# Kernel tuning notes

Measured on AMD Instinct MI355X. Metric: run time of the kernel, lower is better.

## Reference

```python
import jax, jax.numpy as jnp
import numpy as np

BN_EPS = 1e-5
LEAKY_SLOPE = 0.01

N_TOTAL, FEAT_DIM = 100000, 128
N_BATCH, K = 50000, 16
EMBED_DIM = 128


def setup_inputs() -> dict:
    key = jax.random.key(0)
    k1, k2, k3 = jax.random.split(key, 3)
    raw_features = jax.random.normal(k1, (N_TOTAL, FEAT_DIM), dtype=jnp.float32)
    weight = jax.random.normal(k2, (FEAT_DIM, EMBED_DIM), dtype=jnp.float32) * (1.0 / np.sqrt(FEAT_DIM))
    gamma = jnp.ones((EMBED_DIM,), dtype=jnp.float32)
    beta = jnp.zeros((EMBED_DIM,), dtype=jnp.float32)
    neigh_idx = jax.random.randint(k3, (N_BATCH, K), 0, N_TOTAL, dtype=jnp.int64)
    return {"raw_features": raw_features, "weight": weight, "gamma": gamma,
            "beta": beta, "neigh_idx": neigh_idx}


def reference(raw_features, weight, gamma, beta, neigh_idx):
    # Mean aggregation over sampled neighbors: [N_BATCH, K, F] -> [N_BATCH, F]
    neigh_feats = jnp.mean(raw_features[neigh_idx], axis=1)
    # Dense transform: [N_BATCH, EMBED_DIM]
    x = neigh_feats @ weight
    # BatchNorm1d (training mode: batch statistics, biased variance)
    mean = jnp.mean(x, axis=0)
    var = jnp.var(x, axis=0)
    x = (x - mean) * jax.lax.rsqrt(var + BN_EPS) * gamma + beta
    # LeakyReLU (default negative_slope=0.01)
    return jnp.where(x >= 0, x, LEAKY_SLOPE * x)
```

## Files before the change

kernel.cpp:

```cpp
#include <hip/hip_runtime.h>
#include <hip/hip_bf16.h>


#define NTOTAL 100000
#define FEAT   128
#define NB     50000
#define KNEI   16
#define NTILES (NB / 16)

typedef float f32x4 __attribute__((ext_vector_type(4)));
typedef short bf16x8 __attribute__((ext_vector_type(8)));

__device__ __forceinline__ unsigned short f2bf(float f) {
    union { float f; unsigned u; } v; v.f = f;
    unsigned r = v.u + 0x7FFF + ((v.u >> 16) & 1);
    return (unsigned short)(r >> 16);
}

#define WT_LD 136
#define A_LD  136

__global__ __launch_bounds__(256, 4) void enc_gemm(
    const float* __restrict__ raw, const float* __restrict__ W,
    const int* __restrict__ idx, float* __restrict__ out,
    float* __restrict__ gstats)
{
    __shared__ unsigned short sWt[128 * WT_LD];
    __shared__ unsigned short sA[16 * A_LD];
    __shared__ int sidx[256];

    const int t = threadIdx.x;

    #pragma unroll 4
    for (int i = 0; i < 64; ++i) {
        int e = t + i * 256;
        int f = e >> 7, n = e & 127;
        sWt[n * WT_LD + f] = f2bf(W[e]);
    }

    const int lane = t & 63;
    const int wv = t >> 6;
    const int ln = lane & 15;
    const int qd = lane >> 4;
    const int c = t & 31;
    const int g = t >> 5;

    float s1a = 0.f, s2a = 0.f, s1b = 0.f, s2b = 0.f;
    const float4* raw4 = (const float4*)raw;

    for (int tile = blockIdx.x; tile < NTILES; tile += gridDim.x) {
        const int i0 = tile * 16;
        __syncthreads();
        sidx[t] = idx[i0 * KNEI + t];
        __syncthreads();

        #pragma unroll
        for (int rr = 0; rr < 2; ++rr) {
            const int r = g * 2 + rr;
            const int* ip = &sidx[r * KNEI];
            float4 acc = {0.f, 0.f, 0.f, 0.f};
            #pragma unroll
            for (int k = 0; k < KNEI; ++k) {
                float4 v = raw4[(size_t)ip[k] * 32 + c];
                acc.x += v.x; acc.y += v.y; acc.z += v.z; acc.w += v.w;
            }
            ushort4 b;
            b.x = f2bf(acc.x * 0.0625f); b.y = f2bf(acc.y * 0.0625f);
            b.z = f2bf(acc.z * 0.0625f); b.w = f2bf(acc.w * 0.0625f);
            *(ushort4*)&sA[r * A_LD + c * 4] = b;
        }
        __syncthreads();

        f32x4 acc0 = {0.f, 0.f, 0.f, 0.f}, acc1 = {0.f, 0.f, 0.f, 0.f};
        const int n0 = wv * 32 + ln, n1 = n0 + 16;
        #pragma unroll
        for (int kt = 0; kt < 4; ++kt) {
            const int k0 = kt * 32 + qd * 8;
            bf16x8 a  = *(const bf16x8*)&sA[ln * A_LD + k0];
            bf16x8 b0 = *(const bf16x8*)&sWt[n0 * WT_LD + k0];
            bf16x8 b1 = *(const bf16x8*)&sWt[n1 * WT_LD + k0];
            acc0 = __builtin_amdgcn_mfma_f32_16x16x32_bf16(a, b0, acc0, 0, 0, 0);
            acc1 = __builtin_amdgcn_mfma_f32_16x16x32_bf16(a, b1, acc1, 0, 0, 0);
        }

        #pragma unroll
        for (int ri = 0; ri < 4; ++ri) {
            const int row = i0 + qd * 4 + ri;
            float v0 = acc0[ri], v1 = acc1[ri];
            out[row * FEAT + n0] = v0;
            out[row * FEAT + n1] = v1;
            s1a += v0; s2a += v0 * v0;
            s1b += v1; s2b += v1 * v1;
        }
    }

    s1a += __shfl_down(s1a, 32); s1a += __shfl_down(s1a, 16);
    s2a += __shfl_down(s2a, 32); s2a += __shfl_down(s2a, 16);
    s1b += __shfl_down(s1b, 32); s1b += __shfl_down(s1b, 16);
    s2b += __shfl_down(s2b, 32); s2b += __shfl_down(s2b, 16);
    if ((lane >> 4) == 0) {
        const int n0 = wv * 32 + ln, n1 = n0 + 16;
        atomicAdd(&gstats[n0], s1a);
        atomicAdd(&gstats[FEAT + n0], s2a);
        atomicAdd(&gstats[n1], s1b);
        atomicAdd(&gstats[FEAT + n1], s2b);
    }
}

__global__ __launch_bounds__(256) void enc_bn(
    float* __restrict__ out, const float* __restrict__ gstats,
    const float* __restrict__ gamma, const float* __restrict__ beta)
{
    __shared__ float sScale[FEAT], sShift[FEAT];
    const int t = threadIdx.x;
    if (t < FEAT) {
        float s1 = gstats[t], s2 = gstats[FEAT + t];
        float mean = s1 * (1.0f / NB);
        float var = s2 * (1.0f / NB) - mean * mean;
        float sc = gamma[t] * rsqrtf(var + 1e-5f);
        sScale[t] = sc;
        sShift[t] = beta[t] - mean * sc;
    }
    __syncthreads();

    const int total4 = NB * FEAT / 4;
    float4* o4 = (float4*)out;
    for (int e = blockIdx.x * blockDim.x + t; e < total4; e += gridDim.x * blockDim.x) {
        const int f4 = (e & 31) * 4;
        float4 v = o4[e];
        float4 r;
        float y;
        y = v.x * sScale[f4 + 0] + sShift[f4 + 0]; r.x = (y >= 0.f) ? y : 0.01f * y;
        y = v.y * sScale[f4 + 1] + sShift[f4 + 1]; r.y = (y >= 0.f) ? y : 0.01f * y;
        y = v.z * sScale[f4 + 2] + sShift[f4 + 2]; r.z = (y >= 0.f) ? y : 0.01f * y;
        y = v.w * sScale[f4 + 3] + sShift[f4 + 3]; r.w = (y >= 0.f) ? y : 0.01f * y;
        o4[e] = r;
    }
}

extern "C" void kernel_launch(void* const* d_in, const int* in_sizes, int n_in,
                              void* d_out, int out_size, void* d_ws, size_t ws_size,
                              hipStream_t stream) {
    const float* raw   = (const float*)d_in[0];
    const float* W     = (const float*)d_in[1];
    const float* gamma = (const float*)d_in[2];
    const float* beta  = (const float*)d_in[3];
    const int*   idx   = (const int*)d_in[4];
    float* out = (float*)d_out;
    float* gstats = (float*)d_ws;

    hipMemsetAsync(gstats, 0, 2 * FEAT * sizeof(float), stream);
    enc_gemm<<<1024, 256, 0, stream>>>(raw, W, idx, out, gstats);
    enc_bn<<<1024, 256, 0, stream>>>(out, gstats, gamma, beta);
}
```

Baseline: 162.5 us.

## Keep weight fragments in registers, batch gather loads, hoist BN scale

The bf16 weight tile moves out of a 34 KB shared-memory buffer into per-thread register fragments loaded straight from global memory. This cuts LDS use and should allow more resident blocks per CU. The neighbor gather now issues 8 loads at once into two accumulators to expose memory-level parallelism, and the grid grows to 1563 blocks so each block handles about two tiles. The BN kernel hoists per-thread scale and shift into registers, since each thread's feature column stays fixed across its grid-stride loop. In exchange, the per-thread weight loads are strided and uncoalesced and are repeated by every block, and register pressure rises.

Result: slower. 177.5 us (+9.2%).

```diff
diff --git a/kernel.cpp b/kernel.cpp
--- a/kernel.cpp
+++ b/kernel.cpp
@@ -7,6 +7,7 @@
 #define NB     50000
 #define KNEI   16
 #define NTILES (NB / 16)
+#define GRID_A 1563
 
 typedef float f32x4 __attribute__((ext_vector_type(4)));
 typedef short bf16x8 __attribute__((ext_vector_type(8)));
@@ -17,7 +18,6 @@
     return (unsigned short)(r >> 16);
 }
 
-#define WT_LD 136
 #define A_LD  136
 
 __global__ __launch_bounds__(256, 4) void enc_gemm(
@@ -25,25 +25,28 @@
     const int* __restrict__ idx, float* __restrict__ out,
     float* __restrict__ gstats)
 {
-    __shared__ unsigned short sWt[128 * WT_LD];
     __shared__ unsigned short sA[16 * A_LD];
     __shared__ int sidx[256];
 
     const int t = threadIdx.x;
-
-    #pragma unroll 4
-    for (int i = 0; i < 64; ++i) {
-        int e = t + i * 256;
-        int f = e >> 7, n = e & 127;
-        sWt[n * WT_LD + f] = f2bf(W[e]);
-    }
-
     const int lane = t & 63;
     const int wv = t >> 6;
     const int ln = lane & 15;
     const int qd = lane >> 4;
     const int c = t & 31;
     const int g = t >> 5;
+
+    const int n0 = wv * 32 + ln, n1 = n0 + 16;
+    bf16x8 bf0[4], bf1[4];
+    #pragma unroll
+    for (int kt = 0; kt < 4; ++kt) {
+        const int k0 = kt * 32 + qd * 8;
+        #pragma unroll
+        for (int j = 0; j < 8; ++j) {
+            bf0[kt][j] = (short)f2bf(W[(k0 + j) * FEAT + n0]);
+            bf1[kt][j] = (short)f2bf(W[(k0 + j) * FEAT + n1]);
+        }
+    }
 
     float s1a = 0.f, s2a = 0.f, s1b = 0.f, s2b = 0.f;
     const float4* raw4 = (const float4*)raw;
@@ -58,29 +61,37 @@
         for (int rr = 0; rr < 2; ++rr) {
             const int r = g * 2 + rr;
             const int* ip = &sidx[r * KNEI];
-            float4 acc = {0.f, 0.f, 0.f, 0.f};
+            float4 v[8];
+            float ax = 0.f, ay = 0.f, az = 0.f, aw = 0.f;
+            float bx = 0.f, by = 0.f, bz = 0.f, bw = 0.f;
             #pragma unroll
-            for (int k = 0; k < KNEI; ++k) {
-                float4 v = raw4[(size_t)ip[k] * 32 + c];
-                acc.x += v.x; acc.y += v.y; acc.z += v.z; acc.w += v.w;
+            for (int k = 0; k < 8; ++k) v[k] = raw4[(size_t)ip[k] * 32 + c];
+            #pragma unroll
+            for (int k = 0; k < 8; k += 2) {
+                ax += v[k].x;   ay += v[k].y;   az += v[k].z;   aw += v[k].w;
+                bx += v[k+1].x; by += v[k+1].y; bz += v[k+1].z; bw += v[k+1].w;
+            }
+            #pragma unroll
+            for (int k = 0; k < 8; ++k) v[k] = raw4[(size_t)ip[k + 8] * 32 + c];
+            #pragma unroll
+            for (int k = 0; k < 8; k += 2) {
+                ax += v[k].x;   ay += v[k].y;   az += v[k].z;   aw += v[k].w;
+                bx += v[k+1].x; by += v[k+1].y; bz += v[k+1].z; bw += v[k+1].w;
             }
             ushort4 b;
-            b.x = f2bf(acc.x * 0.0625f); b.y = f2bf(acc.y * 0.0625f);
-            b.z = f2bf(acc.z * 0.0625f); b.w = f2bf(acc.w * 0.0625f);
+            b.x = f2bf((ax + bx) * 0.0625f); b.y = f2bf((ay + by) * 0.0625f);
+            b.z = f2bf((az + bz) * 0.0625f); b.w = f2bf((aw + bw) * 0.0625f);
             *(ushort4*)&sA[r * A_LD + c * 4] = b;
         }
         __syncthreads();
 
         f32x4 acc0 = {0.f, 0.f, 0.f, 0.f}, acc1 = {0.f, 0.f, 0.f, 0.f};
-        const int n0 = wv * 32 + ln, n1 = n0 + 16;
         #pragma unroll
         for (int kt = 0; kt < 4; ++kt) {
             const int k0 = kt * 32 + qd * 8;
-            bf16x8 a  = *(const bf16x8*)&sA[ln * A_LD + k0];
-            bf16x8 b0 = *(const bf16x8*)&sWt[n0 * WT_LD + k0];
-            bf16x8 b1 = *(const bf16x8*)&sWt[n1 * WT_LD + k0];
-            acc0 = __builtin_amdgcn_mfma_f32_16x16x32_bf16(a, b0, acc0, 0, 0, 0);
-            acc1 = __builtin_amdgcn_mfma_f32_16x16x32_bf16(a, b1, acc1, 0, 0, 0);
+            bf16x8 a = *(const bf16x8*)&sA[ln * A_LD + k0];
+            acc0 = __builtin_amdgcn_mfma_f32_16x16x32_bf16(a, bf0[kt], acc0, 0, 0, 0);
+            acc1 = __builtin_amdgcn_mfma_f32_16x16x32_bf16(a, bf1[kt], acc1, 0, 0, 0);
         }
 
         #pragma unroll
@@ -98,8 +109,7 @@
     s2a += __shfl_down(s2a, 32); s2a += __shfl_down(s2a, 16);
     s1b += __shfl_down(s1b, 32); s1b += __shfl_down(s1b, 16);
     s2b += __shfl_down(s2b, 32); s2b += __shfl_down(s2b, 16);
-    if ((lane >> 4) == 0) {
-        const int n0 = wv * 32 + ln, n1 = n0 + 16;
+    if (qd == 0) {
         atomicAdd(&gstats[n0], s1a);
         atomicAdd(&gstats[FEAT + n0], s2a);
         atomicAdd(&gstats[n1], s1b);
@@ -123,17 +133,20 @@
     }
     __syncthreads();
 
+    const int f4 = (t & 31) * 4;
+    const float4 sc = *(const float4*)&sScale[f4];
+    const float4 sh = *(const float4*)&sShift[f4];
+
     const int total4 = NB * FEAT / 4;
     float4* o4 = (float4*)out;
     for (int e = blockIdx.x * blockDim.x + t; e < total4; e += gridDim.x * blockDim.x) {
-        const int f4 = (e & 31) * 4;
         float4 v = o4[e];
         float4 r;
         float y;
-        y = v.x * sScale[f4 + 0] + sShift[f4 + 0]; r.x = (y >= 0.f) ? y : 0.01f * y;
-        y = v.y * sScale[f4 + 1] + sShift[f4 + 1]; r.y = (y >= 0.f) ? y : 0.01f * y;
-        y = v.z * sScale[f4 + 2] + sShift[f4 + 2]; r.z = (y >= 0.f) ? y : 0.01f * y;
-        y = v.w * sScale[f4 + 3] + sShift[f4 + 3]; r.w = (y >= 0.f) ? y : 0.01f * y;
+        y = v.x * sc.x + sh.x; r.x = (y >= 0.f) ? y : 0.01f * y;
+        y = v.y * sc.y + sh.y; r.y = (y >= 0.f) ? y : 0.01f * y;
+        y = v.z * sc.z + sh.z; r.z = (y >= 0.f) ? y : 0.01f * y;
+        y = v.w * sc.w + sh.w; r.w = (y >= 0.f) ? y : 0.01f * y;
         o4[e] = r;
     }
 }
@@ -150,6 +163,6 @@
     float* gstats = (float*)d_ws;
 
     hipMemsetAsync(gstats, 0, 2 * FEAT * sizeof(float), stream);
-    enc_gemm<<<1024, 256, 0, stream>>>(raw, W, idx, out, gstats);
+    enc_gemm<<<GRID_A, 256, 0, stream>>>(raw, W, idx, out, gstats);
     enc_bn<<<1024, 256, 0, stream>>>(out, gstats, gamma, beta);
 }
```

## Pre-convert features to bf16 and store intermediate GEMM output as bf16

Applied to the files above, without the earlier changes.

Adds a conversion kernel that casts the full raw feature table and the weight to bf16 in workspace, so the neighbor gather reads half the bytes per row. The GEMM writes its pre-BN output as bf16 to workspace, and the BN kernel reads it back and writes fp32, halving the intermediate round trip. The memset is folded into the conversion kernel. The cost is an extra full pass over the 51 MB feature table, a dependence on workspace size with a fallback path, and extra rounding from summing bf16 inputs.

After: 151.9 us. -6.5%, faster.

```diff
diff --git a/kernel.cpp b/kernel.cpp
--- a/kernel.cpp
+++ b/kernel.cpp
@@ -8,6 +8,12 @@
 #define KNEI   16
 #define NTILES (NB / 16)
 
+#define OFF_STATS 0
+#define OFF_WT    1024
+#define OFF_RAWB  33792
+#define OFF_XB    (33792 + 25600000)
+#define WS_NEEDED (OFF_XB + 12800000)
+
 typedef float f32x4 __attribute__((ext_vector_type(4)));
 typedef short bf16x8 __attribute__((ext_vector_type(8)));
 
@@ -20,7 +26,165 @@
 #define WT_LD 136
 #define A_LD  136
 
-__global__ __launch_bounds__(256, 4) void enc_gemm(
+__global__ __launch_bounds__(256) void enc_conv(
+    const float* __restrict__ raw, const float* __restrict__ W,
+    unsigned short* __restrict__ rawb, unsigned short* __restrict__ Wt,
+    float* __restrict__ gstats)
+{
+    const int t = threadIdx.x;
+    if (blockIdx.x < 64) {
+        int e = blockIdx.x * 256 + t;
+        int n = e >> 7, k = e & 127;
+        Wt[e] = f2bf(W[k * FEAT + n]);
+    }
+    if (blockIdx.x == 64 && t < 2 * FEAT) gstats[t] = 0.f;
+
+    const float4* raw4 = (const float4*)raw;
+    ushort4* rb4 = (ushort4*)rawb;
+    const int NQ = NTOTAL * FEAT / 4;
+    for (int e = blockIdx.x * 256 + t; e < NQ; e += gridDim.x * 256) {
+        float4 v = raw4[e];
+        ushort4 b;
+        b.x = f2bf(v.x); b.y = f2bf(v.y); b.z = f2bf(v.z); b.w = f2bf(v.w);
+        rb4[e] = b;
+    }
+}
+
+__global__ __launch_bounds__(256, 4) void enc_gemm_b(
+    const unsigned short* __restrict__ rawb, const unsigned short* __restrict__ Wt,
+    const int* __restrict__ idx, unsigned short* __restrict__ xb,
+    float* __restrict__ gstats)
+{
+    __shared__ unsigned short sWt[128 * WT_LD];
+    __shared__ unsigned short sA[16 * A_LD];
+    __shared__ int sidx[256];
+
+    const int t = threadIdx.x;
+
+    #pragma unroll
+    for (int i = 0; i < 8; ++i) {
+        int e = t + i * 256;
+        int n = e >> 4, c = e & 15;
+        *(uint4*)&sWt[n * WT_LD + c * 8] = *(const uint4*)&Wt[n * 128 + c * 8];
+    }
+
+    const int lane = t & 63;
+    const int wv = t >> 6;
+    const int ln = lane & 15;
+    const int qd = lane >> 4;
+    const int c2 = t & 15;
+    const int g  = t >> 4;
+    const int n0 = wv * 32 + ln, n1 = n0 + 16;
+
+    float s1a = 0.f, s2a = 0.f, s1b = 0.f, s2b = 0.f;
+
+    for (int tile = blockIdx.x; tile < NTILES; tile += gridDim.x) {
+        const int i0 = tile * 16;
+        __syncthreads();
+        sidx[t] = idx[i0 * KNEI + t];
+        __syncthreads();
+
+        {
+            const int* ip = &sidx[g * KNEI];
+            uint4 v[16];
+            #pragma unroll
+            for (int k = 0; k < KNEI; ++k)
+                v[k] = *(const uint4*)&rawb[(size_t)ip[k] * FEAT + c2 * 8];
+            float a0=0.f,a1=0.f,a2=0.f,a3=0.f,a4=0.f,a5=0.f,a6=0.f,a7=0.f;
+            #pragma unroll
+            for (int k = 0; k < KNEI; ++k) {
+                a0 += __uint_as_float(v[k].x << 16);
+                a1 += __uint_as_float(v[k].x & 0xFFFF0000u);
+                a2 += __uint_as_float(v[k].y << 16);
+                a3 += __uint_as_float(v[k].y & 0xFFFF0000u);
+                a4 += __uint_as_float(v[k].z << 16);
+                a5 += __uint_as_float(v[k].z & 0xFFFF0000u);
+                a6 += __uint_as_float(v[k].w << 16);
+                a7 += __uint_as_float(v[k].w & 0xFFFF0000u);
+            }
+            uint4 b;
+            b.x = (unsigned)f2bf(a0 * 0.0625f) | ((unsigned)f2bf(a1 * 0.0625f) << 16);
+            b.y = (unsigned)f2bf(a2 * 0.0625f) | ((unsigned)f2bf(a3 * 0.0625f) << 16);
+            b.z = (unsigned)f2bf(a4 * 0.0625f) | ((unsigned)f2bf(a5 * 0.0625f) << 16);
+            b.w = (unsigned)f2bf(a6 * 0.0625f) | ((unsigned)f2bf(a7 * 0.0625f) << 16);
+            *(uint4*)&sA[g * A_LD + c2 * 8] = b;
+        }
+        __syncthreads();
+
+        f32x4 acc0 = {0.f, 0.f, 0.f, 0.f}, acc1 = {0.f, 0.f, 0.f, 0.f};
+        #pragma unroll
+        for (int kt = 0; kt < 4; ++kt) {
+            const int k0 = kt * 32 + qd * 8;
+            bf16x8 a  = *(const bf16x8*)&sA[ln * A_LD + k0];
+            bf16x8 b0 = *(const bf16x8*)&sWt[n0 * WT_LD + k0];
+            bf16x8 b1 = *(const bf16x8*)&sWt[n1 * WT_LD + k0];
+            acc0 = __builtin_amdgcn_mfma_f32_16x16x32_bf16(a, b0, acc0, 0, 0, 0);
+            acc1 = __builtin_amdgcn_mfma_f32_16x16x32_bf16(a, b1, acc1, 0, 0, 0);
+        }
+
+        #pragma unroll
+        for (int ri = 0; ri < 4; ++ri) {
+            const int row = i0 + qd * 4 + ri;
+            float v0 = acc0[ri], v1 = acc1[ri];
+            xb[row * FEAT + n0] = f2bf(v0);
+            xb[row * FEAT + n1] = f2bf(v1);
+            s1a += v0; s2a += v0 * v0;
+            s1b += v1; s2b += v1 * v1;
+        }
+    }
+
+    s1a += __shfl_down(s1a, 32); s1a += __shfl_down(s1a, 16);
+    s2a += __shfl_down(s2a, 32); s2a += __shfl_down(s2a, 16);
+    s1b += __shfl_down(s1b, 32); s1b += __shfl_down(s1b, 16);
+    s2b += __shfl_down(s2b, 32); s2b += __shfl_down(s2b, 16);
+    if (qd == 0) {
+        atomicAdd(&gstats[n0], s1a);
+        atomicAdd(&gstats[FEAT + n0], s2a);
+        atomicAdd(&gstats[n1], s1b);
+        atomicAdd(&gstats[FEAT + n1], s2b);
+    }
+}
+
+__global__ __launch_bounds__(256) void enc_bn_b(
+    const unsigned short* __restrict__ xb, float* __restrict__ out,
+    const float* __restrict__ gstats,
+    const float* __restrict__ gamma, const float* __restrict__ beta)
+{
+    __shared__ float sScale[FEAT], sShift[FEAT];
+    const int t = threadIdx.x;
+    if (t < FEAT) {
+        float s1 = gstats[t], s2 = gstats[FEAT + t];
+        float mean = s1 * (1.0f / NB);
+        float var = s2 * (1.0f / NB) - mean * mean;
+        float sc = gamma[t] * rsqrtf(var + 1e-5f);
+        sScale[t] = sc;
+        sShift[t] = beta[t] - mean * sc;
+    }
+    __syncthreads();
+
+    const int f8 = (t & 15) * 8;
+    const float4 sc0 = *(const float4*)&sScale[f8], sc1 = *(const float4*)&sScale[f8 + 4];
+    const float4 sh0 = *(const float4*)&sShift[f8], sh1 = *(const float4*)&sShift[f8 + 4];
+
+    const uint4* x4 = (const uint4*)xb;
+    float4* o4 = (float4*)out;
+    const int total8 = NB * FEAT / 8;
+    for (int e = blockIdx.x * 256 + t; e < total8; e += gridDim.x * 256) {
+        uint4 v = x4[e];
+        float4 r0, r1; float y;
+        y = __uint_as_float(v.x << 16)        * sc0.x + sh0.x; r0.x = (y >= 0.f) ? y : 0.01f * y;
+        y = __uint_as_float(v.x & 0xFFFF0000u)* sc0.y + sh0.y; r0.y = (y >= 0.f) ? y : 0.01f * y;
+        y = __uint_as_float(v.y << 16)        * sc0.z + sh0.z; r0.z = (y >= 0.f) ? y : 0.01f * y;
+        y = __uint_as_float(v.y & 0xFFFF0000u)* sc0.w + sh0.w; r0.w = (y >= 0.f) ? y : 0.01f * y;
+        y = __uint_as_float(v.z << 16)        * sc1.x + sh1.x; r1.x = (y >= 0.f) ? y : 0.01f * y;
+        y = __uint_as_float(v.z & 0xFFFF0000u)* sc1.y + sh1.y; r1.y = (y >= 0.f) ? y : 0.01f * y;
+        y = __uint_as_float(v.w << 16)        * sc1.z + sh1.z; r1.z = (y >= 0.f) ? y : 0.01f * y;
+        y = __uint_as_float(v.w & 0xFFFF0000u)* sc1.w + sh1.w; r1.w = (y >= 0.f) ? y : 0.01f * y;
+        o4[e * 2] = r0; o4[e * 2 + 1] = r1;
+    }
+}
+
+__global__ __launch_bounds__(256, 4) void enc_gemm_f(
     const float* __restrict__ raw, const float* __restrict__ W,
     const int* __restrict__ idx, float* __restrict__ out,
     float* __restrict__ gstats)
@@ -28,32 +192,23 @@
     __shared__ unsigned short sWt[128 * WT_LD];
     __shared__ unsigned short sA[16 * A_LD];
     __shared__ int sidx[256];
-
-    const int t = threadIdx.x;
-
+    const int t = threadIdx.x;
     #pragma unroll 4
     for (int i = 0; i < 64; ++i) {
         int e = t + i * 256;
         int f = e >> 7, n = e & 127;
         sWt[n * WT_LD + f] = f2bf(W[e]);
     }
-
-    const int lane = t & 63;
-    const int wv = t >> 6;
-    const int ln = lane & 15;
-    const int qd = lane >> 4;
-    const int c = t & 31;
-    const int g = t >> 5;
-
+    const int lane = t & 63, wv = t >> 6, ln = lane & 15, qd = lane >> 4;
+    const int c = t & 31, g = t >> 5;
+    const int n0 = wv * 32 + ln, n1 = n0 + 16;
     float s1a = 0.f, s2a = 0.f, s1b = 0.f, s2b = 0.f;
     const float4* raw4 = (const float4*)raw;
-
     for (int tile = blockIdx.x; tile < NTILES; tile += gridDim.x) {
         const int i0 = tile * 16;
         __syncthreads();
         sidx[t] = idx[i0 * KNEI + t];
         __syncthreads();
-
         #pragma unroll
         for (int rr = 0; rr < 2; ++rr) {
             const int r = g * 2 + rr;
@@ -70,9 +225,7 @@
             *(ushort4*)&sA[r * A_LD + c * 4] = b;
         }
         __syncthreads();
-
         f32x4 acc0 = {0.f, 0.f, 0.f, 0.f}, acc1 = {0.f, 0.f, 0.f, 0.f};
-        const int n0 = wv * 32 + ln, n1 = n0 + 16;
         #pragma unroll
         for (int kt = 0; kt < 4; ++kt) {
             const int k0 = kt * 32 + qd * 8;
@@ -82,7 +235,6 @@
             acc0 = __builtin_amdgcn_mfma_f32_16x16x32_bf16(a, b0, acc0, 0, 0, 0);
             acc1 = __builtin_amdgcn_mfma_f32_16x16x32_bf16(a, b1, acc1, 0, 0, 0);
         }
-
         #pragma unroll
         for (int ri = 0; ri < 4; ++ri) {
             const int row = i0 + qd * 4 + ri;
@@ -93,13 +245,11 @@
             s1b += v1; s2b += v1 * v1;
         }
     }
-
     s1a += __shfl_down(s1a, 32); s1a += __shfl_down(s1a, 16);
     s2a += __shfl_down(s2a, 32); s2a += __shfl_down(s2a, 16);
     s1b += __shfl_down(s1b, 32); s1b += __shfl_down(s1b, 16);
     s2b += __shfl_down(s2b, 32); s2b += __shfl_down(s2b, 16);
-    if ((lane >> 4) == 0) {
-        const int n0 = wv * 32 + ln, n1 = n0 + 16;
+    if (qd == 0) {
         atomicAdd(&gstats[n0], s1a);
         atomicAdd(&gstats[FEAT + n0], s2a);
         atomicAdd(&gstats[n1], s1b);
@@ -107,7 +257,7 @@
     }
 }
 
-__global__ __launch_bounds__(256) void enc_bn(
+__global__ __launch_bounds__(256) void enc_bn_f(
     float* __restrict__ out, const float* __restrict__ gstats,
     const float* __restrict__ gamma, const float* __restrict__ beta)
 {
@@ -122,18 +272,18 @@
         sShift[t] = beta[t] - mean * sc;
     }
     __syncthreads();
-
+    const int f4 = (t & 31) * 4;
+    const float4 sc = *(const float4*)&sScale[f4];
+    const float4 sh = *(const float4*)&sShift[f4];
     const int total4 = NB * FEAT / 4;
     float4* o4 = (float4*)out;
-    for (int e = blockIdx.x * blockDim.x + t; e < total4; e += gridDim.x * blockDim.x) {
-        const int f4 = (e & 31) * 4;
+    for (int e = blockIdx.x * 256 + t; e < total4; e += gridDim.x * 256) {
         float4 v = o4[e];
-        float4 r;
-        float y;
-        y = v.x * sScale[f4 + 0] + sShift[f4 + 0]; r.x = (y >= 0.f) ? y : 0.01f * y;
-        y = v.y * sScale[f4 + 1] + sShift[f4 + 1]; r.y = (y >= 0.f) ? y : 0.01f * y;
-        y = v.z * sScale[f4 + 2] + sShift[f4 + 2]; r.z = (y >= 0.f) ? y : 0.01f * y;
-        y = v.w * sScale[f4 + 3] + sShift[f4 + 3]; r.w = (y >= 0.f) ? y : 0.01f * y;
+        float4 r; float y;
+        y = v.x * sc.x + sh.x; r.x = (y >= 0.f) ? y : 0.01f * y;
+        y = v.y * sc.y + sh.y; r.y = (y >= 0.f) ? y : 0.01f * y;
+        y = v.z * sc.z + sh.z; r.z = (y >= 0.f) ? y : 0.01f * y;
+        y = v.w * sc.w + sh.w; r.w = (y >= 0.f) ? y : 0.01f * y;
         o4[e] = r;
     }
 }
@@ -147,9 +297,20 @@
     const float* beta  = (const float*)d_in[3];
     const int*   idx   = (const int*)d_in[4];
     float* out = (float*)d_out;
-    float* gstats = (float*)d_ws;
-
-    hipMemsetAsync(gstats, 0, 2 * FEAT * sizeof(float), stream);
-    enc_gemm<<<1024, 256, 0, stream>>>(raw, W, idx, out, gstats);
-    enc_bn<<<1024, 256, 0, stream>>>(out, gstats, gamma, beta);
-}
+
+    char* ws = (char*)d_ws;
+    float* gstats = (float*)(ws + OFF_STATS);
+
+    if (ws_size >= WS_NEEDED) {
+        unsigned short* Wt   = (unsigned short*)(ws + OFF_WT);
+        unsigned short* rawb = (unsigned short*)(ws + OFF_RAWB);
+        unsigned short* xb   = (unsigned short*)(ws + OFF_XB);
+        enc_conv<<<2048, 256, 0, stream>>>(raw, W, rawb, Wt, gstats);
+        enc_gemm_b<<<1024, 256, 0, stream>>>(rawb, Wt, idx, xb, gstats);
+        enc_bn_b<<<1024, 256, 0, stream>>>(xb, out, gstats, gamma, beta);
+    } else {
+        hipMemsetAsync(gstats, 0, 2 * FEAT * sizeof(float), stream);
+        enc_gemm_f<<<1024, 256, 0, stream>>>(raw, W, idx, out, gstats);
+        enc_bn_f<<<1024, 256, 0, stream>>>(out, gstats, gamma, beta);
+    }
+}
```
